# Optimization experiments

Measured on AMD Instinct MI355X. Metric: run time of the kernel, lower is better.

Reference implementation:

```python
import jax, jax.numpy as jnp
import numpy as np

D_MODEL = 1024
NUM_HEADS = 16
D_K = D_MODEL // NUM_HEADS


def setup_inputs() -> dict:
    key = jax.random.key(0)
    ks = jax.random.split(key, 11)
    B, S = 2, 2048
    scale = 1.0 / np.sqrt(D_MODEL)
    return {
        "Q": jax.random.normal(ks[0], (B, S, D_MODEL), jnp.float32),
        "K": jax.random.normal(ks[1], (B, S, D_MODEL), jnp.float32),
        "V": jax.random.normal(ks[2], (B, S, D_MODEL), jnp.float32),
        "Wq": jax.random.normal(ks[3], (D_MODEL, D_MODEL), jnp.float32) * scale,
        "bq": jnp.zeros((D_MODEL,), jnp.float32),
        "Wk": jax.random.normal(ks[4], (D_MODEL, D_MODEL), jnp.float32) * scale,
        "bk": jnp.zeros((D_MODEL,), jnp.float32),
        "Wv": jax.random.normal(ks[5], (D_MODEL, D_MODEL), jnp.float32) * scale,
        "bv": jnp.zeros((D_MODEL,), jnp.float32),
        "Wo": jax.random.normal(ks[6], (D_MODEL, D_MODEL), jnp.float32) * scale,
        "bo": jnp.zeros((D_MODEL,), jnp.float32),
    }


def reference(Q, K, V, Wq, bq, Wk, bk, Wv, bv, Wo, bo):
    B, S, _ = Q.shape
    # linear projections (torch Linear: x @ W.T + b)
    q = Q @ Wq.T + bq
    k = K @ Wk.T + bk
    v = V @ Wv.T + bv
    # split heads: [B, S, H, d_k] -> [B, H, S, d_k]
    q = q.reshape(B, S, NUM_HEADS, D_K).transpose(0, 2, 1, 3)
    k = k.reshape(B, S, NUM_HEADS, D_K).transpose(0, 2, 1, 3)
    v = v.reshape(B, S, NUM_HEADS, D_K).transpose(0, 2, 1, 3)
    # scaled dot-product attention, full [B, H, S, S] scores as in original
    scores = jnp.einsum("bhqd,bhkd->bhqk", q, k) / jnp.sqrt(jnp.float32(D_K))
    probs = jax.nn.softmax(scores, axis=-1)
    attn = jnp.einsum("bhqk,bhkd->bhqd", probs, v)
    # merge heads and output projection
    attn = attn.transpose(0, 2, 1, 3).reshape(B, S, D_MODEL)
    return attn @ Wo.T + bo
```

## Files before the change

kernel.cpp:

```cpp
#include <hip/hip_runtime.h>
#include <cstdint>
#include <cstddef>

#define D_MODEL 1024
#define NHEADS 16
#define DK 64
#define BATCH 2
#define SEQ 2048
#define MROWS 4096

using f32x4 = __attribute__((ext_vector_type(4))) float;
using f32x16 = __attribute__((ext_vector_type(16))) float;
using u16x8 = __attribute__((ext_vector_type(8))) unsigned short;
using u32x4 = __attribute__((ext_vector_type(4))) unsigned int;
using bf16x8 = __attribute__((ext_vector_type(8))) __bf16;

static __device__ __forceinline__ f32x4 mfma16(u16x8 a, u16x8 b, f32x4 c) {
    return __builtin_amdgcn_mfma_f32_16x16x32_bf16(
        __builtin_bit_cast(bf16x8, a), __builtin_bit_cast(bf16x8, b), c, 0, 0, 0);
}
static __device__ __forceinline__ f32x16 mfma32(u16x8 a, u16x8 b, f32x16 c) {
    return __builtin_amdgcn_mfma_f32_32x32x16_bf16(
        __builtin_bit_cast(bf16x8, a), __builtin_bit_cast(bf16x8, b), c, 0, 0, 0);
}

static __device__ __forceinline__ unsigned short f2b(float f) {
    unsigned int u = __float_as_uint(f);
    u += 0x7fffu + ((u >> 16) & 1u);
    return (unsigned short)(u >> 16);
}
static __device__ __forceinline__ unsigned int cvt_pk(float lo, float hi) {
    unsigned int r;
    asm("v_cvt_pk_bf16_f32 %0, %1, %2" : "=v"(r) : "v"(lo), "v"(hi));
    return r;
}
static __device__ __forceinline__ void plswap(unsigned int& a, unsigned int& b) {
    asm("v_permlane32_swap_b32 %0, %1" : "+v"(a), "+v"(b));
}
static __device__ __forceinline__ float fexp2(float x) {
#if __has_builtin(__builtin_amdgcn_exp2f)
    return __builtin_amdgcn_exp2f(x);
#else
    float r;
    asm("v_exp_f32 %0, %1" : "=v"(r) : "v"(x));
    return r;
#endif
}
static __device__ __forceinline__ void gll16(const void* g, void* l) {
    __builtin_amdgcn_global_load_lds(
        (const __attribute__((address_space(1))) void*)g,
        (__attribute__((address_space(3))) void*)l, 16, 0, 0);
}
#define SBAR() __builtin_amdgcn_s_barrier()
#define SCHED0() __builtin_amdgcn_sched_barrier(0)
#define WAITV(n) asm volatile("s_waitcnt vmcnt(" #n ")" ::: "memory")
#define WAITL0() asm volatile("s_waitcnt lgkmcnt(0)" ::: "memory")

__global__ __launch_bounds__(256) void cvtw_kernel(const float* __restrict__ w0,
                                                   const float* __restrict__ w1,
                                                   const float* __restrict__ w2,
                                                   const float* __restrict__ w3,
                                                   unsigned short* __restrict__ out,
                                                   int n4, float scale0) {
    const float* srcs[4] = {w0, w1, w2, w3};
    const float* src = srcs[blockIdx.y];
    unsigned short* dst = out + (size_t)blockIdx.y * (size_t)n4 * 4;
    float scale = (blockIdx.y == 0) ? scale0 : 1.0f;
    int i = blockIdx.x * 256 + threadIdx.x;
    if (i < n4) {
        float4 v = reinterpret_cast<const float4*>(src)[i];
        ushort4 o;
        o.x = f2b(v.x * scale);
        o.y = f2b(v.y * scale);
        o.z = f2b(v.z * scale);
        o.w = f2b(v.w * scale);
        reinterpret_cast<ushort4*>(dst)[i] = o;
    }
}


struct AReg { float4 r0, r1, r2, r3; };

__global__ __launch_bounds__(256, 3) void gemm_qkv_kernel(
    const float* __restrict__ A0, const float* __restrict__ A1, const float* __restrict__ A2,
    const unsigned short* __restrict__ W,
    unsigned short* __restrict__ qo, unsigned short* __restrict__ ko,
    unsigned short* __restrict__ vto,
    const float* __restrict__ b0, const float* __restrict__ b1, const float* __restrict__ b2,
    float qsc) {
    __shared__ __align__(16) char Asb[8192];
    __shared__ __align__(16) char Wb[2][8192];

    const int tid = threadIdx.x;
    const int lane = tid & 63;
    const int wid = tid >> 6;
    const int wr = wid >> 1, wc = wid & 1;
    const int g = (lane >> 4) & 3, l16 = lane & 15;

    const int logical = ((int)blockIdx.x & 7) * 96 + ((int)blockIdx.x >> 3);
    const int m = logical >> 8;
    const int rem = logical & 255;
    const int y = rem >> 3, xc = rem & 7;
    const int row0 = y * 128;
    const int wrow0 = m * 1024 + xc * 128;

    const float* Af = (m == 0) ? A0 : ((m == 1) ? A1 : A2);

    const int arow = tid >> 1;
    const int ahalf = tid & 1;
    const float* asrc = Af + (size_t)(row0 + arow) * 1024 + ahalf * 16;
    const int aline = tid >> 2;
    const int apar = (tid >> 1) & 1;
    const int al7 = aline & 7;
    const int aglo = ((apar * 4 + ahalf * 2) ^ al7) * 16;
    const int aghi = ((apar * 4 + ahalf * 2 + 1) ^ al7) * 16;

    const int sline = tid >> 3;
    const int sgl = (tid & 7) ^ (sline & 7);
    const int srow = sline * 2 + (sgl >> 2);
    const int skcol = (sgl & 3) * 8;

    AReg rA, rB;
    auto loadTo = [&](AReg& R, int k0) {
        const float4* s = reinterpret_cast<const float4*>(asrc + k0);
        R.r0 = s[0];
        R.r1 = s[1];
        R.r2 = s[2];
        R.r3 = s[3];
    };
    auto writeFrom = [&](AReg& R) {
        u32x4 glo = {cvt_pk(R.r0.x, R.r0.y), cvt_pk(R.r0.z, R.r0.w),
                     cvt_pk(R.r1.x, R.r1.y), cvt_pk(R.r1.z, R.r1.w)};
        u32x4 ghi = {cvt_pk(R.r2.x, R.r2.y), cvt_pk(R.r2.z, R.r2.w),
                     cvt_pk(R.r3.x, R.r3.y), cvt_pk(R.r3.z, R.r3.w)};
        *reinterpret_cast<u32x4*>(Asb + aline * 128 + aglo) = glo;
        *reinterpret_cast<u32x4*>(Asb + aline * 128 + aghi) = ghi;
    };
    auto stageW = [&](int k0, int buf) {
        const char* w0 = (const char*)W + (size_t)(wrow0 + srow) * 2048 + (size_t)(k0 + skcol) * 2;
        gll16(w0, Wb[buf] + wid * 1024);
        gll16(w0 + (size_t)64 * 2048, Wb[buf] + 4096 + wid * 1024);
    };

    const int rswz = ((((l16 & 1) << 2) + g) ^ ((l16 >> 1) & 7)) << 4;
    const int abase = (wr * 32 + (l16 >> 1)) * 128 + rswz;
    const int bbase = (wc * 32 + (l16 >> 1)) * 128 + rswz;

    f32x4 acc[4][4] = {};

    loadTo(rA, 0);
    loadTo(rB, 32);
    stageW(0, 0);
    stageW(32, 1);
    WAITV(8);
    SCHED0();
    writeFrom(rA);
    WAITL0();
    SCHED0();

    auto iter = [&](int t, AReg& ld, AReg& wr_) {
        if (t < 30) loadTo(ld, (t + 2) * 32);
        if (t == 0) WAITV(6);
        else if (t < 30) WAITV(10);
        else if (t == 30) WAITV(6);
        else WAITV(0);
        SCHED0();
        SBAR();
        SCHED0();
        u16x8 af[4], bf[4];
#pragma unroll
        for (int mi = 0; mi < 4; ++mi)
            af[mi] = *reinterpret_cast<const u16x8*>(Asb + abase + mi * 1024);
#pragma unroll
        for (int ni = 0; ni < 4; ++ni)
            bf[ni] = *reinterpret_cast<const u16x8*>(Wb[t & 1] + bbase + ni * 1024);
        __builtin_amdgcn_s_setprio(1);
#pragma unroll
        for (int mi = 0; mi < 4; ++mi)
#pragma unroll
            for (int ni = 0; ni < 4; ++ni)
                acc[mi][ni] = mfma16(af[mi], bf[ni], acc[mi][ni]);
        __builtin_amdgcn_s_setprio(0);
        if (t < 31) {
            SBAR();
            SCHED0();
            if (t < 30) stageW((t + 2) * 32, t & 1);
            if (t < 30) WAITV(8);
            else WAITV(2);
            SCHED0();
            writeFrom(wr_);
            WAITL0();
            SCHED0();
        }
    };
#pragma unroll 1
    for (int tt = 0; tt < 16; ++tt) {
        iter(2 * tt, rA, rB);
        iter(2 * tt + 1, rB, rA);
    }

    const float* bias = (m == 0) ? b0 : ((m == 1) ? b1 : b2);
    const float bsc = (m == 0) ? qsc : 1.0f;
#pragma unroll
    for (int mi = 0; mi < 4; ++mi) {
#pragma unroll
        for (int ni = 0; ni < 4; ++ni) {
            int r = row0 + wr * 64 + mi * 16 + g * 4;
            int cl = xc * 128 + wc * 64 + ni * 16 + l16;
            float bv = bsc * bias[cl];
            if (m < 2) {
                unsigned short* outp = m ? ko : qo;
#pragma unroll
                for (int j = 0; j < 4; ++j)
                    outp[(size_t)(r + j) * 1024 + cl] = f2b(acc[mi][ni][j] + bv);
            } else {
                ushort4 o;
                o.x = f2b(acc[mi][ni][0] + bv);
                o.y = f2b(acc[mi][ni][1] + bv);
                o.z = f2b(acc[mi][ni][2] + bv);
                o.w = f2b(acc[mi][ni][3] + bv);
                *reinterpret_cast<ushort4*>(vto + (size_t)cl * MROWS + r) = o;
            }
        }
    }
}

__global__ __launch_bounds__(256, 4) void gemm_out_kernel(
    const unsigned short* __restrict__ Abf,
    const unsigned short* __restrict__ W,
    float* __restrict__ fo,
    const float* __restrict__ bias) {
    __shared__ __align__(16) char Ab[2][8192];
    __shared__ __align__(16) char Wb[2][4096];

    const int tid = threadIdx.x;
    const int lane = tid & 63;
    const int wid = tid >> 6;
    const int wr = wid >> 1, wc = wid & 1;
    const int g = (lane >> 4) & 3, l16 = lane & 15;

    const int logical = ((int)blockIdx.x & 7) * 64 + ((int)blockIdx.x >> 3);
    const int y = logical >> 4, xc = logical & 15;
    const int row0 = y * 128;
    const int wrow0 = xc * 64;

    const int sline = tid >> 3;
    const int sgl = (tid & 7) ^ (sline & 7);
    const int srow = sline * 2 + (sgl >> 2);
    const int skcol = (sgl & 3) * 8;

    auto stage = [&](int k0, int buf) {
        const char* a0 = (const char*)Abf + (size_t)(row0 + srow) * 2048 + (size_t)(k0 + skcol) * 2;
        gll16(a0, Ab[buf] + wid * 1024);
        gll16(a0 + (size_t)64 * 2048, Ab[buf] + 4096 + wid * 1024);
        const char* w0 = (const char*)W + (size_t)(wrow0 + srow) * 2048 + (size_t)(k0 + skcol) * 2;
        gll16(w0, Wb[buf] + wid * 1024);
    };

    const int rswz = ((((l16 & 1) << 2) + g) ^ ((l16 >> 1) & 7)) << 4;
    const int abase = (wr * 32 + (l16 >> 1)) * 128 + rswz;
    const int bbase = (wc * 16 + (l16 >> 1)) * 128 + rswz;

    f32x4 acc[4][2] = {};
    stage(0, 0);

    for (int t = 0; t < 32; ++t) {
        if (t < 31) stage((t + 1) * 32, (t & 1) ^ 1);
        if (t < 31) WAITV(3);
        else WAITV(0);
        SCHED0();
        SBAR();
        SCHED0();
        u16x8 af[4], bf[2];
#pragma unroll
        for (int mi = 0; mi < 4; ++mi)
            af[mi] = *reinterpret_cast<const u16x8*>(Ab[t & 1] + abase + mi * 1024);
#pragma unroll
        for (int ni = 0; ni < 2; ++ni)
            bf[ni] = *reinterpret_cast<const u16x8*>(Wb[t & 1] + bbase + ni * 1024);
        __builtin_amdgcn_s_setprio(1);
#pragma unroll
        for (int mi = 0; mi < 4; ++mi)
#pragma unroll
            for (int ni = 0; ni < 2; ++ni)
                acc[mi][ni] = mfma16(af[mi], bf[ni], acc[mi][ni]);
        __builtin_amdgcn_s_setprio(0);
        SBAR();
        SCHED0();
    }

#pragma unroll
    for (int mi = 0; mi < 4; ++mi) {
#pragma unroll
        for (int ni = 0; ni < 2; ++ni) {
            int r = row0 + wr * 64 + mi * 16 + g * 4;
            int cl = xc * 64 + wc * 32 + ni * 16 + l16;
            float bv = bias[cl];
#pragma unroll
            for (int j = 0; j < 4; ++j)
                fo[(size_t)(r + j) * 1024 + cl] = acc[mi][ni][j] + bv;
        }
    }
}

__global__ __launch_bounds__(512, 2) void attn_kernel(
    const unsigned short* __restrict__ qp,
    const unsigned short* __restrict__ kp,
    const unsigned short* __restrict__ vT,
    unsigned short* __restrict__ ao) {
    __shared__ __align__(16) char lds[36864];

    const int tid = threadIdx.x;
    const int lane = tid & 63;
    const int wid = tid >> 6;
    const int wq = wid & 3, wk = wid >> 2;
    const int l31 = lane & 31, hi = lane >> 5;

    const int logical = ((int)blockIdx.x & 7) * 64 + ((int)blockIdx.x >> 3);
    const int qt = logical & 15;
    const int bh = logical >> 4;
    const int b = bh >> 4, h = bh & 15;
    const int ch = h * DK;
    const int q0 = b * SEQ + qt * 128;

    const int kline = tid >> 3;
    const int krow = kline & 31;
    const int kgl = (tid & 7) ^ (krow & 7);
    const char* ksrc = (const char*)kp +
        ((size_t)(b * SEQ + (kline >> 5) * 1024 + krow)) * 2048 + ch * 2 + kgl * 16;
    const int vd = tid >> 3;
    const int vgl = (tid & 7) ^ (vd & 7);
    const char* vsrc = (const char*)vT + ((size_t)(ch + vd)) * (MROWS * 2) +
        ((size_t)(b * SEQ + (vgl >> 2) * 1024 + (vgl & 3) * 8)) * 2;

    const char* qr = (const char*)qp + (size_t)(q0 + wq * 32 + l31) * 2048 + ch * 2;
    u16x8 qf[4];
#pragma unroll
    for (int t = 0; t < 4; ++t)
        qf[t] = *reinterpret_cast<const u16x8*>(qr + t * 32 + hi * 16);

    auto stageKV = [&](int kt2, char* base) {
        gll16(ksrc + (size_t)kt2 * 65536, base + wid * 1024);
        gll16(vsrc + kt2 * 64, base + 8192 + wid * 1024);
    };

    const int sw7 = (l31 & 7);
    f32x16 acco[2] = {};
    float l0 = 0.f, l1 = 0.f, l2 = 0.f, l3 = 0.f;

    stageKV(0, lds);
    for (int kt = 0; kt < 32; ++kt) {
        if (kt < 31) {
            stageKV(kt + 1, lds + (((kt + 1) & 1) << 14));
            WAITV(2);
        } else {
            WAITV(0);
        }
        SCHED0();
        SBAR();
        SCHED0();
        const char* cb = lds + ((kt & 1) << 14);

        f32x16 s = {};
        __builtin_amdgcn_s_setprio(1);
#pragma unroll
        for (int t = 0; t < 4; ++t) {
            u16x8 kf = *reinterpret_cast<const u16x8*>(
                cb + wk * 4096 + l31 * 128 + (((2 * t + hi) ^ sw7) << 4));
            s = mfma32(kf, qf[t], s);
        }
        __builtin_amdgcn_s_setprio(0);

        float p[16];
#pragma unroll
        for (int r = 0; r < 16; r += 4) {
            p[r] = fexp2(s[r]);
            p[r + 1] = fexp2(s[r + 1]);
            p[r + 2] = fexp2(s[r + 2]);
            p[r + 3] = fexp2(s[r + 3]);
            l0 += p[r];
            l1 += p[r + 1];
            l2 += p[r + 2];
            l3 += p[r + 3];
        }
        unsigned int pf0[4], pf1[4];
#pragma unroll
        for (int i = 0; i < 2; ++i) {
            unsigned int a = cvt_pk(p[2 * i], p[2 * i + 1]);
            unsigned int bb = cvt_pk(p[4 + 2 * i], p[5 + 2 * i]);
            plswap(a, bb);
            pf0[i] = a;
            pf0[i + 2] = bb;
            unsigned int a2 = cvt_pk(p[8 + 2 * i], p[9 + 2 * i]);
            unsigned int b2 = cvt_pk(p[12 + 2 * i], p[13 + 2 * i]);
            plswap(a2, b2);
            pf1[i] = a2;
            pf1[i + 2] = b2;
        }

        __builtin_amdgcn_s_setprio(1);
#pragma unroll
        for (int t = 0; t < 2; ++t) {
            u32x4 wv = t ? u32x4{pf1[0], pf1[1], pf1[2], pf1[3]}
                         : u32x4{pf0[0], pf0[1], pf0[2], pf0[3]};
            u16x8 pfr = __builtin_bit_cast(u16x8, wv);
#pragma unroll
            for (int dt = 0; dt < 2; ++dt) {
                u16x8 vf = *reinterpret_cast<const u16x8*>(
                    cb + 8192 + (dt * 32 + l31) * 128 + (((wk * 4 + 2 * t + hi) ^ sw7) << 4));
                acco[dt] = mfma32(vf, pfr, acco[dt]);
            }
        }
        __builtin_amdgcn_s_setprio(0);
        SBAR();
        SCHED0();
    }

    float L = (l0 + l1) + (l2 + l3);

    float Lh = L + __shfl_xor(L, 32);
    float* cmb = reinterpret_cast<float*>(lds);
    float* slot = cmb + (size_t)tid * 18;
    f32x16 outg = acco[1 ^ wk];
#pragma unroll
    for (int mm = 0; mm < 8; ++mm)
        *reinterpret_cast<float2*>(slot + 2 * mm) = float2{outg[2 * mm], outg[2 * mm + 1]};
    slot[16] = Lh;
    __syncthreads();
    const float* ps = cmb + (size_t)(tid ^ 256) * 18;
    f32x16 kept = acco[wk];
#pragma unroll
    for (int mm = 0; mm < 8; ++mm) {
        float2 t2 = *reinterpret_cast<const float2*>(ps + 2 * mm);
        kept[2 * mm] += t2.x;
        kept[2 * mm + 1] += t2.y;
    }
    float rl = 1.0f / (Lh + ps[16]);
    __syncthreads();

    char* ot = lds + wid * 2304;
    const int r7 = l31 & 7;
#pragma unroll
    for (int mm = 0; mm < 4; ++mm) {
        uint2 pko;
        pko.x = cvt_pk(kept[4 * mm] * rl, kept[4 * mm + 1] * rl);
        pko.y = cvt_pk(kept[4 * mm + 2] * rl, kept[4 * mm + 3] * rl);
        *reinterpret_cast<uint2*>(ot + l31 * 72 + (((2 * mm + hi) ^ r7) << 3)) = pko;
    }
    const int rr = lane >> 1, half = lane & 1;
    const int rb7 = rr & 7;
    uint2 t0 = *reinterpret_cast<const uint2*>(ot + rr * 72 + (((half * 4 + 0) ^ rb7) << 3));
    uint2 t1 = *reinterpret_cast<const uint2*>(ot + rr * 72 + (((half * 4 + 1) ^ rb7) << 3));
    uint2 t2 = *reinterpret_cast<const uint2*>(ot + rr * 72 + (((half * 4 + 2) ^ rb7) << 3));
    uint2 t3 = *reinterpret_cast<const uint2*>(ot + rr * 72 + (((half * 4 + 3) ^ rb7) << 3));
    unsigned short* dst = ao + (size_t)(q0 + wq * 32 + rr) * 1024 + ch + wk * 32 + half * 16;
    uint4 o0 = {t0.x, t0.y, t1.x, t1.y};
    uint4 o1 = {t2.x, t2.y, t3.x, t3.y};
    *reinterpret_cast<uint4*>(dst) = o0;
    *reinterpret_cast<uint4*>(dst + 8) = o1;
}

extern "C" void kernel_launch(void* const* d_in, const int* in_sizes, int n_in,
                              void* d_out, int out_size, void* d_ws, size_t ws_size,
                              hipStream_t stream) {
    const float* Q = (const float*)d_in[0];
    const float* K = (const float*)d_in[1];
    const float* V = (const float*)d_in[2];
    const float* Wq = (const float*)d_in[3];
    const float* bq = (const float*)d_in[4];
    const float* Wk = (const float*)d_in[5];
    const float* bk = (const float*)d_in[6];
    const float* Wv = (const float*)d_in[7];
    const float* bv = (const float*)d_in[8];
    const float* Wo = (const float*)d_in[9];
    const float* bo = (const float*)d_in[10];

    unsigned short* ws = (unsigned short*)d_ws;
    const size_t SZ = (size_t)MROWS * D_MODEL;
    const size_t WSZ = (size_t)D_MODEL * D_MODEL;
    unsigned short* bufW = ws;
    unsigned short* qp = bufW + 4 * WSZ;
    unsigned short* kp = qp + SZ;
    unsigned short* vT = kp + SZ;
    unsigned short* ao = vT + SZ;

    const float qscale = 0.125f * 1.44269504088896f;

    dim3 blk(256);
    dim3 gcw((unsigned)(WSZ / 4 / 256), 4);
    cvtw_kernel<<<gcw, blk, 0, stream>>>(Wq, Wk, Wv, Wo, bufW, (int)(WSZ / 4), qscale);

    gemm_qkv_kernel<<<dim3(768), blk, 0, stream>>>(Q, K, V, bufW, qp, kp, vT, bq, bk, bv, qscale);

    attn_kernel<<<dim3(512), dim3(512), 0, stream>>>(qp, kp, vT, ao);

    gemm_out_kernel<<<dim3(512), blk, 0, stream>>>(ao, bufW + 3 * WSZ, (float*)d_out, bo);
}
```

Baseline: 127.5 us.

## Pre-convert activations to bf16 and stage both GEMM operands via direct LDS loads

```diff
diff --git a/kernel.cpp b/kernel.cpp
--- a/kernel.cpp
+++ b/kernel.cpp
@@ -54,18 +54,28 @@
 #define SBAR() __builtin_amdgcn_s_barrier()
 #define SCHED0() __builtin_amdgcn_sched_barrier(0)
 #define WAITV(n) asm volatile("s_waitcnt vmcnt(" #n ")" ::: "memory")
-#define WAITL0() asm volatile("s_waitcnt lgkmcnt(0)" ::: "memory")
-
-__global__ __launch_bounds__(256) void cvtw_kernel(const float* __restrict__ w0,
-                                                   const float* __restrict__ w1,
-                                                   const float* __restrict__ w2,
-                                                   const float* __restrict__ w3,
-                                                   unsigned short* __restrict__ out,
-                                                   int n4, float scale0) {
-    const float* srcs[4] = {w0, w1, w2, w3};
-    const float* src = srcs[blockIdx.y];
-    unsigned short* dst = out + (size_t)blockIdx.y * (size_t)n4 * 4;
-    float scale = (blockIdx.y == 0) ? scale0 : 1.0f;
+
+__global__ __launch_bounds__(256) void cvt_all_kernel(
+    const float* __restrict__ w0, const float* __restrict__ w1,
+    const float* __restrict__ w2, const float* __restrict__ w3,
+    const float* __restrict__ a0, const float* __restrict__ a1,
+    const float* __restrict__ a2,
+    unsigned short* __restrict__ outW, unsigned short* __restrict__ outA,
+    int n4w, int n4a, float scale0) {
+    const float* srcs[7] = {w0, w1, w2, w3, a0, a1, a2};
+    const int y = blockIdx.y;
+    const float* src = srcs[y];
+    unsigned short* dst;
+    int n4;
+    float scale = 1.0f;
+    if (y < 4) {
+        dst = outW + (size_t)y * (size_t)n4w * 4;
+        n4 = n4w;
+        if (y == 0) scale = scale0;
+    } else {
+        dst = outA + (size_t)(y - 4) * (size_t)n4a * 4;
+        n4 = n4a;
+    }
     int i = blockIdx.x * 256 + threadIdx.x;
     if (i < n4) {
         float4 v = reinterpret_cast<const float4*>(src)[i];
@@ -79,16 +89,14 @@
 }
 
 
-struct AReg { float4 r0, r1, r2, r3; };
-
-__global__ __launch_bounds__(256, 3) void gemm_qkv_kernel(
-    const float* __restrict__ A0, const float* __restrict__ A1, const float* __restrict__ A2,
+__global__ __launch_bounds__(256, 4) void gemm_qkv_kernel(
+    const unsigned short* __restrict__ Abf,
     const unsigned short* __restrict__ W,
     unsigned short* __restrict__ qo, unsigned short* __restrict__ ko,
     unsigned short* __restrict__ vto,
     const float* __restrict__ b0, const float* __restrict__ b1, const float* __restrict__ b2,
     float qsc) {
-    __shared__ __align__(16) char Asb[8192];
+    __shared__ __align__(16) char Ab[2][8192];
     __shared__ __align__(16) char Wb[2][8192];
 
     const int tid = threadIdx.x;
@@ -102,41 +110,18 @@
     const int rem = logical & 255;
     const int y = rem >> 3, xc = rem & 7;
     const int row0 = y * 128;
+    const int arow0 = m * MROWS + row0;
     const int wrow0 = m * 1024 + xc * 128;
-
-    const float* Af = (m == 0) ? A0 : ((m == 1) ? A1 : A2);
-
-    const int arow = tid >> 1;
-    const int ahalf = tid & 1;
-    const float* asrc = Af + (size_t)(row0 + arow) * 1024 + ahalf * 16;
-    const int aline = tid >> 2;
-    const int apar = (tid >> 1) & 1;
-    const int al7 = aline & 7;
-    const int aglo = ((apar * 4 + ahalf * 2) ^ al7) * 16;
-    const int aghi = ((apar * 4 + ahalf * 2 + 1) ^ al7) * 16;
 
     const int sline = tid >> 3;
     const int sgl = (tid & 7) ^ (sline & 7);
     const int srow = sline * 2 + (sgl >> 2);
     const int skcol = (sgl & 3) * 8;
 
-    AReg rA, rB;
-    auto loadTo = [&](AReg& R, int k0) {
-        const float4* s = reinterpret_cast<const float4*>(asrc + k0);
-        R.r0 = s[0];
-        R.r1 = s[1];
-        R.r2 = s[2];
-        R.r3 = s[3];
-    };
-    auto writeFrom = [&](AReg& R) {
-        u32x4 glo = {cvt_pk(R.r0.x, R.r0.y), cvt_pk(R.r0.z, R.r0.w),
-                     cvt_pk(R.r1.x, R.r1.y), cvt_pk(R.r1.z, R.r1.w)};
-        u32x4 ghi = {cvt_pk(R.r2.x, R.r2.y), cvt_pk(R.r2.z, R.r2.w),
-                     cvt_pk(R.r3.x, R.r3.y), cvt_pk(R.r3.z, R.r3.w)};
-        *reinterpret_cast<u32x4*>(Asb + aline * 128 + aglo) = glo;
-        *reinterpret_cast<u32x4*>(Asb + aline * 128 + aghi) = ghi;
-    };
-    auto stageW = [&](int k0, int buf) {
+    auto stage = [&](int k0, int buf) {
+        const char* a0 = (const char*)Abf + (size_t)(arow0 + srow) * 2048 + (size_t)(k0 + skcol) * 2;
+        gll16(a0, Ab[buf] + wid * 1024);
+        gll16(a0 + (size_t)64 * 2048, Ab[buf] + 4096 + wid * 1024);
         const char* w0 = (const char*)W + (size_t)(wrow0 + srow) * 2048 + (size_t)(k0 + skcol) * 2;
         gll16(w0, Wb[buf] + wid * 1024);
         gll16(w0 + (size_t)64 * 2048, Wb[buf] + 4096 + wid * 1024);
@@ -147,22 +132,11 @@
     const int bbase = (wc * 32 + (l16 >> 1)) * 128 + rswz;
 
     f32x4 acc[4][4] = {};
-
-    loadTo(rA, 0);
-    loadTo(rB, 32);
-    stageW(0, 0);
-    stageW(32, 1);
-    WAITV(8);
-    SCHED0();
-    writeFrom(rA);
-    WAITL0();
-    SCHED0();
-
-    auto iter = [&](int t, AReg& ld, AReg& wr_) {
-        if (t < 30) loadTo(ld, (t + 2) * 32);
-        if (t == 0) WAITV(6);
-        else if (t < 30) WAITV(10);
-        else if (t == 30) WAITV(6);
+    stage(0, 0);
+
+    for (int t = 0; t < 32; ++t) {
+        if (t < 31) stage((t + 1) * 32, (t & 1) ^ 1);
+        if (t < 31) WAITV(4);
         else WAITV(0);
         SCHED0();
         SBAR();
@@ -170,7 +144,7 @@
         u16x8 af[4], bf[4];
 #pragma unroll
         for (int mi = 0; mi < 4; ++mi)
-            af[mi] = *reinterpret_cast<const u16x8*>(Asb + abase + mi * 1024);
+            af[mi] = *reinterpret_cast<const u16x8*>(Ab[t & 1] + abase + mi * 1024);
 #pragma unroll
         for (int ni = 0; ni < 4; ++ni)
             bf[ni] = *reinterpret_cast<const u16x8*>(Wb[t & 1] + bbase + ni * 1024);
@@ -181,22 +155,8 @@
             for (int ni = 0; ni < 4; ++ni)
                 acc[mi][ni] = mfma16(af[mi], bf[ni], acc[mi][ni]);
         __builtin_amdgcn_s_setprio(0);
-        if (t < 31) {
-            SBAR();
-            SCHED0();
-            if (t < 30) stageW((t + 2) * 32, t & 1);
-            if (t < 30) WAITV(8);
-            else WAITV(2);
-            SCHED0();
-            writeFrom(wr_);
-            WAITL0();
-            SCHED0();
-        }
-    };
-#pragma unroll 1
-    for (int tt = 0; tt < 16; ++tt) {
-        iter(2 * tt, rA, rB);
-        iter(2 * tt + 1, rB, rA);
+        SBAR();
+        SCHED0();
     }
 
     const float* bias = (m == 0) ? b0 : ((m == 1) ? b1 : b2);
@@ -479,7 +439,8 @@
     const size_t SZ = (size_t)MROWS * D_MODEL;
     const size_t WSZ = (size_t)D_MODEL * D_MODEL;
     unsigned short* bufW = ws;
-    unsigned short* qp = bufW + 4 * WSZ;
+    unsigned short* abf = bufW + 4 * WSZ;
+    unsigned short* qp = abf + 3 * SZ;
     unsigned short* kp = qp + SZ;
     unsigned short* vT = kp + SZ;
     unsigned short* ao = vT + SZ;
@@ -487,10 +448,11 @@
     const float qscale = 0.125f * 1.44269504088896f;
 
     dim3 blk(256);
-    dim3 gcw((unsigned)(WSZ / 4 / 256), 4);
-    cvtw_kernel<<<gcw, blk, 0, stream>>>(Wq, Wk, Wv, Wo, bufW, (int)(WSZ / 4), qscale);
-
-    gemm_qkv_kernel<<<dim3(768), blk, 0, stream>>>(Q, K, V, bufW, qp, kp, vT, bq, bk, bv, qscale);
+    dim3 gcv((unsigned)(SZ / 4 / 256), 7);
+    cvt_all_kernel<<<gcv, blk, 0, stream>>>(Wq, Wk, Wv, Wo, Q, K, V, bufW, abf,
+                                            (int)(WSZ / 4), (int)(SZ / 4), qscale);
+
+    gemm_qkv_kernel<<<dim3(768), blk, 0, stream>>>(abf, bufW, qp, kp, vT, bq, bk, bv, qscale);
 
     attn_kernel<<<dim3(512), dim3(512), 0, stream>>>(qp, kp, vT, ao);
 
```

After: 128.3 us. About the same (+0.6%).
